# Kernel tuning notes

Measured on AMD Instinct MI355X. Metric: run time of the kernel, lower is better.

## Reference

```python
import jax, jax.numpy as jnp
import numpy as np

V, D, U, L, B, T = 32000, 256, 512, 2, 16, 128


def _lstm_stack(x, mask, params):
    """Stacked LSTM over time-major x [T,B,D] with mask [T,B].
    Keras LSTMCell gate order i,f,g,o; masked steps carry previous h,c."""
    nb = x.shape[1]
    init = tuple((jnp.zeros((nb, U), x.dtype), jnp.zeros((nb, U), x.dtype)) for _ in params)

    def step(carry, inp):
        xt, mt = inp
        m = mt[:, None]
        new = []
        h_in = xt
        for (W, Uw, b), (h, c) in zip(params, carry):
            z = h_in @ W + h @ Uw + b          # [B, 4U]
            i, f, g, o = jnp.split(z, 4, axis=-1)
            c_new = jax.nn.sigmoid(f) * c + jax.nn.sigmoid(i) * jnp.tanh(g)
            h_new = jax.nn.sigmoid(o) * jnp.tanh(c_new)
            h_new = jnp.where(m, h_new, h)
            c_new = jnp.where(m, c_new, c)
            new.append((h_new, c_new))
            h_in = h_new
        return tuple(new), h_in

    _, ys = jax.lax.scan(step, init, (x, mask))
    return ys  # [T, B, U]


def setup_inputs() -> dict:
    key = jax.random.key(0)
    ks = jax.random.split(key, 16)
    s = 0.05
    seqs = jax.random.randint(ks[0], (B, T), 0, V)
    embed = jax.random.normal(ks[1], (V, D), dtype=jnp.float32) * 0.01

    def lstm_p(k, din):
        k1, k2 = jax.random.split(k)
        return (jax.random.normal(k1, (din, 4 * U), dtype=jnp.float32) * s,
                jax.random.normal(k2, (U, 4 * U), dtype=jnp.float32) * s,
                jnp.zeros((4 * U,), dtype=jnp.float32))

    fW0, fU0, fb0 = lstm_p(ks[2], D)
    fW1, fU1, fb1 = lstm_p(ks[3], U)
    bW0, bU0, bb0 = lstm_p(ks[4], D)
    bW1, bU1, bb1 = lstm_p(ks[5], U)
    Wp = jax.random.normal(ks[6], (2 * U, V), dtype=jnp.float32) * s
    bp = jnp.zeros((V,), dtype=jnp.float32)
    return {"seqs": seqs, "embed": embed,
            "fW0": fW0, "fU0": fU0, "fb0": fb0, "fW1": fW1, "fU1": fU1, "fb1": fb1,
            "bW0": bW0, "bU0": bU0, "bb0": bb0, "bW1": bW1, "bU1": bU1, "bb1": bb1,
            "Wp": Wp, "bp": bp}


def reference(seqs, embed, fW0, fU0, fb0, fW1, fU1, fb1,
              bW0, bU0, bb0, bW1, bU1, bb1, Wp, bp):
    emb = embed[seqs]                      # [B, T, D]
    mask = seqs != 0                       # mask_zero=True
    # forward LSTM over tokens 0..T-2
    fx = jnp.swapaxes(emb[:, :-1], 0, 1)   # [T-1, B, D]
    fm = jnp.swapaxes(mask[:, :-1], 0, 1)
    f = jnp.swapaxes(_lstm_stack(fx, fm, [(fW0, fU0, fb0), (fW1, fU1, fb1)]), 0, 1)  # [B,T-1,U]
    # backward LSTM (go_backwards): process tokens 1..T-1 reversed in time
    bx = jnp.swapaxes(emb[:, 1:][:, ::-1], 0, 1)
    bm = jnp.swapaxes(mask[:, 1:][:, ::-1], 0, 1)
    b = jnp.swapaxes(_lstm_stack(bx, bm, [(bW0, bU0, bb0), (bW1, bU1, bb1)]), 0, 1)  # reversed-time order
    b_rev = b[:, ::-1]                     # tf.reverse(b, axis=[1]) -> natural order
    o = jnp.concatenate([f[:, :-1], b_rev[:, 1:]], axis=-1)  # [B, T-2, 2U]
    word_logits = o @ Wp + bp              # [B, T-2, V]
    return word_logits
```

## Files before the change

kernel.cpp:

```cpp
#include <hip/hip_runtime.h>

#define VOCAB 32000
#define DIM   256
#define UN    512
#define TT    128
#define T1    126
#define NG    2048
#define NBLK  256

typedef __attribute__((ext_vector_type(8))) __bf16 bf16x8;
typedef __attribute__((ext_vector_type(4))) float  f32x4;

__device__ __forceinline__ unsigned short f2bf(float f) {
  union { float f; unsigned u; } v; v.f = f;
  unsigned r = (v.u + 0x7fffu + ((v.u >> 16) & 1u)) >> 16;
  return (unsigned short)r;
}
__device__ __forceinline__ float f4_get(const float4& v, int j) {
  return j == 0 ? v.x : j == 1 ? v.y : j == 2 ? v.z : v.w;
}
__device__ __forceinline__ void async16(const void* g, void* l) {
  __builtin_amdgcn_global_load_lds((const __attribute__((address_space(1))) void*)g,
                                   (__attribute__((address_space(3))) void*)l, 16, 0, 0);
}

__global__ __launch_bounds__(256) void k_gather(const int* __restrict__ seqs,
                                                const float* __restrict__ embed,
                                                float* __restrict__ emb) {
  int idx = blockIdx.x * 256 + threadIdx.x;
  int d4 = idx & 63, bt = idx >> 6;
  int tok = seqs[bt];
  ((float4*)emb)[idx] = ((const float4*)embed)[(size_t)tok * 64 + d4];
}

__global__ __launch_bounds__(256, 2) void k_zin(const float* __restrict__ emb,
    const float* __restrict__ fW0, const float* __restrict__ fb0,
    const float* __restrict__ bW0, const float* __restrict__ bb0,
    float* __restrict__ Z0) {
  __shared__ __align__(16) float xs[16 * 260];
  int bi = blockIdx.x;
  int jh  = bi & 1;
  int t   = (bi >> 1) % T1;
  int dir = (bi >> 1) / T1;
  int tim = dir ? (TT - 1) - t : t;
  const float* W    = dir ? bW0 : fW0;
  const float* bias = dir ? bb0 : fb0;
  int tid = threadIdx.x;
  #pragma unroll
  for (int i = 0; i < 4; ++i) {
    int fidx = i * 256 + tid;
    int b = fidx >> 6, k4 = fidx & 63;
    float4 v = ((const float4*)emb)[(size_t)(b * TT + tim) * 64 + k4];
    *(float4*)&xs[b * 260 + k4 * 4] = v;
  }
  __syncthreads();
  int j0 = jh * 1024 + tid;
  float acc[4][16];
  #pragma unroll
  for (int q = 0; q < 4; ++q) {
    float bv = bias[j0 + q * 256];
    #pragma unroll
    for (int b = 0; b < 16; ++b) acc[q][b] = bv;
  }
  #pragma unroll 2
  for (int k = 0; k < DIM; k += 4) {
    float4 xv[16];
    #pragma unroll
    for (int b = 0; b < 16; ++b) xv[b] = *(const float4*)&xs[b * 260 + k];
    #pragma unroll
    for (int kk = 0; kk < 4; ++kk) {
      float w[4];
      #pragma unroll
      for (int q = 0; q < 4; ++q) w[q] = W[(size_t)(k + kk) * NG + j0 + q * 256];
      #pragma unroll
      for (int q = 0; q < 4; ++q)
        #pragma unroll
        for (int b = 0; b < 16; ++b)
          acc[q][b] += f4_get(xv[b], kk) * w[q];
    }
  }
  float* out = Z0 + ((size_t)(dir * T1 + t) * 16) * NG;
  #pragma unroll
  for (int q = 0; q < 4; ++q)
    #pragma unroll
    for (int b = 0; b < 16; ++b)
      out[(size_t)b * NG + j0 + q * 256] = acc[q][b];
}

__global__ __launch_bounds__(256) void k_cast_wp(const float* __restrict__ Wp,
                                                 unsigned short* __restrict__ Bt) {
  __shared__ float tile[32][33];
  int bi = blockIdx.x;
  int kt = bi & 31, nt = bi >> 5;
  int k0 = kt * 32, n0 = nt * 32;
  int tid = threadIdx.x;
  int nl = tid & 31, kl = tid >> 5;
  #pragma unroll
  for (int i = 0; i < 4; ++i) {
    int k = kl + i * 8;
    tile[k][nl] = Wp[(size_t)(k0 + k) * VOCAB + n0 + nl];
  }
  __syncthreads();
  int kl2 = tid & 31, nl2 = tid >> 5;
  #pragma unroll
  for (int i = 0; i < 4; ++i) {
    int n = nl2 + i * 8;
    Bt[(size_t)(n0 + n) * 1024 + k0 + kl2] = f2bf(tile[kl2][n]);
  }
}

__global__ __launch_bounds__(256) void k_padA(unsigned short* __restrict__ A) {
  int idx = blockIdx.x * 256 + threadIdx.x;
  ((uint4*)(A + (size_t)2016 * 1024))[idx] = make_uint4(0u, 0u, 0u, 0u);
}


__device__ __forceinline__ void wait_epoch(const int* ep, int target) {
  if (threadIdx.x == 0) {
    while (__hip_atomic_load(ep, __ATOMIC_RELAXED, __HIP_MEMORY_SCOPE_AGENT) < target)
      __builtin_amdgcn_s_sleep(2);
  }
  __syncthreads();
}

__device__ __forceinline__ void signal_step(int* grp, int sub_idx, int s) {
  __builtin_amdgcn_s_waitcnt(0);
  __syncthreads();
  if (threadIdx.x == 0) {
    int old = __hip_atomic_fetch_add(grp + sub_idx * 32, 1,
                                     __ATOMIC_RELAXED, __HIP_MEMORY_SCOPE_AGENT);
    if (old == 8 * (s + 1) - 1) {
      int mold = __hip_atomic_fetch_add(grp + 256, 1,
                                        __ATOMIC_RELAXED, __HIP_MEMORY_SCOPE_AGENT);
      if (mold == 8 * (s + 1) - 1) {
        #pragma unroll
        for (int i = 0; i < 8; ++i)
          __hip_atomic_store(grp + 512 + i * 32, s + 1,
                             __ATOMIC_RELAXED, __HIP_MEMORY_SCOPE_AGENT);
      }
    }
  }
}

__device__ __forceinline__ void ldstage_regs(float4 (&v)[8], const float* __restrict__ src) {
  const int tid = threadIdx.x;
  #pragma unroll
  for (int i = 0; i < 8; ++i) {
    const int fidx = i * 256 + tid;
    const int b = fidx >> 7, k = (fidx & 127) * 4;
    v[i] = *(const float4*)&src[(size_t)b * 512 + k];
  }
}
__device__ __forceinline__ void ldswrite(float* xs, const float4 (&v)[8]) {
  const int tid = threadIdx.x;
  #pragma unroll
  for (int i = 0; i < 8; ++i) {
    const int fidx = i * 256 + tid;
    const int b = fidx >> 7, k = (fidx & 127) * 4;
    *(float4*)&xs[b * 640 + (k >> 4) * 20 + (k & 15)] = v[i];
  }
}

__device__ __forceinline__ void phase_acc(const float* xs, const float (&u)[4][16],
                                          float (&acc)[4][16], int kp) {
  const float* xb = xs + kp * 20;
  #pragma unroll
  for (int kk4 = 0; kk4 < 4; ++kk4) {
    float4 xv[16];
    #pragma unroll
    for (int b = 0; b < 16; ++b) xv[b] = *(const float4*)&xb[b * 640 + kk4 * 4];
    #pragma unroll
    for (int j = 0; j < 4; ++j)
      #pragma unroll
      for (int g = 0; g < 4; ++g) {
        float uv = u[g][kk4 * 4 + j];
        #pragma unroll
        for (int b = 0; b < 16; ++b) acc[g][b] += f4_get(xv[b], j) * uv;
      }
  }
}

template <int LAYER>
__device__ void recur_path(const int* __restrict__ seqs,
                           const float* __restrict__ Z0,
                           const float* __restrict__ P1,
                           const float* __restrict__ P2,
                           const float* __restrict__ b1,
                           float* __restrict__ H0,
                           float* __restrict__ h1,
                           unsigned short* __restrict__ A,
                           int* grp_own, int sub_idx,
                           const int* ep_own, const int* ep_l0,
                           float* xsA, float* xsB, float* red,
                           int dir, int u0)
{
  const int tid = threadIdx.x;
  const int kp = tid >> 3;
  const int unit = u0 + (tid & 7);
  float u1r[4][16], u2r[4][16];
  #pragma unroll
  for (int g = 0; g < 4; ++g)
    #pragma unroll
    for (int kk = 0; kk < 16; ++kk) {
      const int col = g * UN + unit;
      u1r[g][kk] = P1[(size_t)(kp * 16 + kk) * NG + col];
      if (LAYER) u2r[g][kk] = P2[(size_t)(kp * 16 + kk) * NG + col];
    }
  const int cu = tid & 7, cb = tid >> 3;
  const int un = u0 + cu;
  float b1r[4] = {0.f, 0.f, 0.f, 0.f};
  if (LAYER && tid < 128) {
    #pragma unroll
    for (int g = 0; g < 4; ++g) b1r[g] = b1[g * UN + un];
  }
  float hst = 0.f, cstate = 0.f;

  for (int t = 0; t < 126; ++t) {
    float zp[4] = {0.f, 0.f, 0.f, 0.f};
    bool m = false;
    if (tid < 128) {
      const int tim = dir ? (TT - 1) - t : t;
      m = seqs[cb * TT + tim] != 0;
      if (LAYER == 0) {
        const float* zr = Z0 + (((size_t)dir * T1 + t) * 16 + cb) * NG;
        #pragma unroll
        for (int g = 0; g < 4; ++g) zp[g] = zr[g * UN + un];
      }
    }
    if (LAYER == 0) {
      float4 va[8];
      if (t == 0) {
        #pragma unroll
        for (int i = 0; i < 8; ++i) va[i] = make_float4(0.f, 0.f, 0.f, 0.f);
      } else {
        wait_epoch(ep_own, t);
        ldstage_regs(va, H0 + ((size_t)(dir * T1 + (t - 1)) * 16) * UN);
      }
      ldswrite(xsA, va);
    } else {
      float4 va[8], vb[8];
      if (t >= 1) {
        wait_epoch(ep_own, t);
        ldstage_regs(vb, h1 + ((size_t)((t - 1) * 2 + dir) * 16) * UN);
      } else {
        #pragma unroll
        for (int i = 0; i < 8; ++i) vb[i] = make_float4(0.f, 0.f, 0.f, 0.f);
      }
      wait_epoch(ep_l0, t + 1);
      ldstage_regs(va, H0 + ((size_t)(dir * T1 + t) * 16) * UN);
      ldswrite(xsB, vb);
      ldswrite(xsA, va);
    }
    __syncthreads();

    float acc[4][16];
    #pragma unroll
    for (int g = 0; g < 4; ++g)
      #pragma unroll
      for (int b = 0; b < 16; ++b) acc[g][b] = 0.f;
    phase_acc(xsA, u1r, acc, kp);
    if (LAYER) phase_acc(xsB, u2r, acc, kp);

    #pragma unroll
    for (int g = 0; g < 4; ++g)
      #pragma unroll
      for (int b = 0; b < 16; ++b) {
        float v = acc[g][b];
        v += __shfl_xor(v, 8);
        v += __shfl_xor(v, 16);
        v += __shfl_xor(v, 32);
        acc[g][b] = v;
      }
    const int lane = tid & 63, wv = tid >> 6;
    if (lane < 8) {
      #pragma unroll
      for (int g = 0; g < 4; ++g)
        #pragma unroll
        for (int b = 0; b < 16; ++b)
          red[((wv * 8 + lane) * 4 + g) * 17 + b] = acc[g][b];
    }
    __syncthreads();

    if (tid < 128) {
      float z[4];
      #pragma unroll
      for (int g = 0; g < 4; ++g) {
        float v = red[(cu * 4 + g) * 17 + cb];
        #pragma unroll
        for (int w = 1; w < 4; ++w) v += red[((w * 8 + cu) * 4 + g) * 17 + cb];
        z[g] = v + (LAYER ? b1r[g] : zp[g]);
      }
      const float si = 1.f / (1.f + expf(-z[0]));
      const float sf = 1.f / (1.f + expf(-z[1]));
      const float tg = tanhf(z[2]);
      const float so = 1.f / (1.f + expf(-z[3]));
      const float cn = sf * cstate + si * tg;
      const float hn = so * tanhf(cn);
      const float hsel = m ? hn : hst;
      const float csel = m ? cn : cstate;
      cstate = csel; hst = hsel;
      if (LAYER == 0) {
        __hip_atomic_store(&H0[(((size_t)dir * T1 + t) * 16 + cb) * UN + un],
                           hsel, __ATOMIC_RELAXED, __HIP_MEMORY_SCOPE_AGENT);
      } else {
        __hip_atomic_store(&h1[(((size_t)t * 2 + dir) * 16 + cb) * UN + un],
                           hsel, __ATOMIC_RELAXED, __HIP_MEMORY_SCOPE_AGENT);
        const int row = dir ? (125 - t) : t;
        A[((size_t)cb * T1 + row) * 1024 + dir * UN + un] = f2bf(hsel);
      }
    }
    signal_step(grp_own, sub_idx, t);
  }
}

__global__ __launch_bounds__(256, 1) void k_recur(
    const int* __restrict__ seqs, const float* __restrict__ Z0,
    const float* __restrict__ fU0, const float* __restrict__ bU0,
    const float* __restrict__ fW1, const float* __restrict__ fU1, const float* __restrict__ fb1,
    const float* __restrict__ bW1, const float* __restrict__ bU1, const float* __restrict__ bb1,
    float* __restrict__ H0, float* __restrict__ h1, unsigned short* __restrict__ A,
    int* __restrict__ bar)
{
  __shared__ __align__(16) float xs[2][16 * 640];
  __shared__ float red[32 * 4 * 17];
  const int bi = blockIdx.x;
  const int dir = (bi >> 6) & 1;
  const int u0 = (bi & 63) * 8;
  const int gid = bi >> 6;
  int* grp_own = bar + gid * 1024;
  const int* ep_own = grp_own + 512 + (bi & 7) * 32;
  const int* ep_l0  = bar + dir * 1024 + 512 + (bi & 7) * 32;
  if ((bi >> 7) == 0)
    recur_path<0>(seqs, Z0, dir ? bU0 : fU0, nullptr, nullptr,
                  H0, h1, A, grp_own, bi & 7, ep_own, ep_l0,
                  xs[0], xs[1], red, dir, u0);
  else
    recur_path<1>(seqs, Z0, dir ? bW1 : fW1, dir ? bU1 : fU1, dir ? bb1 : fb1,
                  H0, h1, A, grp_own, bi & 7, ep_own, ep_l0,
                  xs[0], xs[1], red, dir, u0);
}

__global__ __launch_bounds__(256, 2) void k_proj(
    const unsigned short* __restrict__ Abf, const unsigned short* __restrict__ Bt,
    const float* __restrict__ bp, float* __restrict__ out)
{
  __shared__ unsigned short As[128 * 32];
  __shared__ unsigned short Bs[128 * 32];
  int bi = blockIdx.x;
  int mt = bi & 15, nt = bi >> 4;
  int m0 = mt * 128, n0 = nt * 128;
  int tid = threadIdx.x;
  int wv = tid >> 6, lane = tid & 63;
  int wm = wv & 1, wn = wv >> 1;
  f32x4 acc[4][4] = {};
  for (int kt = 0; kt < 32; ++kt) {
    int r0 = wv * 32;
    #pragma unroll
    for (int i = 0; i < 2; ++i) {
      int row = r0 + i * 16 + (lane >> 2);
      const unsigned short* ga = Abf + (size_t)(m0 + row) * 1024 + kt * 32 + (lane & 3) * 8;
      async16(ga, As + (r0 + i * 16) * 32);
      const unsigned short* gb = Bt + (size_t)(n0 + row) * 1024 + kt * 32 + (lane & 3) * 8;
      async16(gb, Bs + (r0 + i * 16) * 32);
    }
    __syncthreads();
    bf16x8 af[4], bf[4];
    #pragma unroll
    for (int i = 0; i < 4; ++i) {
      int m = wm * 64 + i * 16 + (lane & 15);
      af[i] = *(const bf16x8*)&As[m * 32 + (lane >> 4) * 8];
      int n = wn * 64 + i * 16 + (lane & 15);
      bf[i] = *(const bf16x8*)&Bs[n * 32 + (lane >> 4) * 8];
    }
    #pragma unroll
    for (int i = 0; i < 4; ++i)
      #pragma unroll
      for (int j = 0; j < 4; ++j)
        acc[i][j] = __builtin_amdgcn_mfma_f32_16x16x32_bf16(af[i], bf[j], acc[i][j], 0, 0, 0);
    __syncthreads();
  }
  #pragma unroll
  for (int j = 0; j < 4; ++j) {
    int col = n0 + wn * 64 + j * 16 + (lane & 15);
    float bv = bp[col];
    #pragma unroll
    for (int i = 0; i < 4; ++i) {
      int rbase = m0 + wm * 64 + i * 16 + (lane >> 4) * 4;
      #pragma unroll
      for (int r = 0; r < 4; ++r) {
        int row = rbase + r;
        if (row < 2016) out[(size_t)row * VOCAB + col] = acc[i][j][r] + bv;
      }
    }
  }
}

extern "C" void kernel_launch(void* const* d_in, const int* in_sizes, int n_in,
                              void* d_out, int out_size, void* d_ws, size_t ws_size,
                              hipStream_t stream)
{
  const int*   seqs  = (const int*)  d_in[0];
  const float* embed = (const float*)d_in[1];
  const float* fW0 = (const float*)d_in[2];
  const float* fU0 = (const float*)d_in[3];
  const float* fb0 = (const float*)d_in[4];
  const float* fW1 = (const float*)d_in[5];
  const float* fU1 = (const float*)d_in[6];
  const float* fb1 = (const float*)d_in[7];
  const float* bW0 = (const float*)d_in[8];
  const float* bU0 = (const float*)d_in[9];
  const float* bb0 = (const float*)d_in[10];
  const float* bW1 = (const float*)d_in[11];
  const float* bU1 = (const float*)d_in[12];
  const float* bb1 = (const float*)d_in[13];
  const float* Wp  = (const float*)d_in[14];
  const float* bp  = (const float*)d_in[15];
  float* out = (float*)d_out;

  char* ws = (char*)d_ws;
  float* emb   = (float*)(ws);
  float* Z0    = (float*)(ws + 2097152);
  float* H0    = (float*)(ws + 35127296);
  float* h1    = (float*)(ws + 43384832);
  unsigned short* A  = (unsigned short*)(ws + 51642368);
  unsigned short* Bt = (unsigned short*)(ws + 55836672);
  int* bar = (int*)(ws + 1048576);

  hipLaunchKernelGGL(k_gather, dim3(512), dim3(256), 0, stream, seqs, embed, emb);
  hipLaunchKernelGGL(k_zin, dim3(504), dim3(256), 0, stream, emb, fW0, fb0, bW0, bb0, Z0);
  hipLaunchKernelGGL(k_cast_wp, dim3(32000), dim3(256), 0, stream, Wp, Bt);
  hipLaunchKernelGGL(k_padA, dim3(16), dim3(256), 0, stream, A);
  hipMemsetAsync(bar, 0, 16384, stream);

  void* rargs[] = {(void*)&seqs, (void*)&Z0, (void*)&fU0, (void*)&bU0,
                   (void*)&fW1, (void*)&fU1, (void*)&fb1,
                   (void*)&bW1, (void*)&bU1, (void*)&bb1,
                   (void*)&H0, (void*)&h1, (void*)&A, (void*)&bar};
  hipError_t ce = hipLaunchCooperativeKernel((void*)k_recur, dim3(NBLK), dim3(256),
                                             rargs, 0, stream);
  if (ce != hipSuccess) {
    (void)hipGetLastError();
    hipLaunchKernelGGL(k_recur, dim3(NBLK), dim3(256), 0, stream,
                       seqs, Z0, fU0, bU0, fW1, fU1, fb1, bW1, bU1, bb1,
                       H0, h1, A, bar);
  }

  hipLaunchKernelGGL(k_proj, dim3(4000), dim3(256), 0, stream, A, Bt, bp, out);
}
```

Before: 2.088 ms.

## Fold layer-0 and layer-1 LSTM chains into 128 blocks with flat counters

The persistent recurrence kernel drops from 256 to 128 blocks. Each block now runs the layer-0 step for one direction and the layer-1 step for the other direction in the same time loop, holding three weight slices in registers. The two-level barrier counter (per-subgroup, then master) becomes a single 64-way counter per chain, and the spin-wait sleep is shortened. The aim is to cut barrier latency and participant count per step, at the cost of serialising two cell updates per block per step and raising register pressure.

After: 3.540 ms. +69.5%, slower.

```diff
diff --git a/kernel.cpp b/kernel.cpp
--- a/kernel.cpp
+++ b/kernel.cpp
@@ -6,7 +6,7 @@
 #define TT    128
 #define T1    126
 #define NG    2048
-#define NBLK  256
+#define NBLK  128
 
 typedef __attribute__((ext_vector_type(8))) __bf16 bf16x8;
 typedef __attribute__((ext_vector_type(4))) float  f32x4;
@@ -115,29 +115,36 @@
 }
 
 
-__device__ __forceinline__ void wait_epoch(const int* ep, int target) {
+__device__ __forceinline__ void wait1(const int* ep, int tgt) {
   if (threadIdx.x == 0) {
-    while (__hip_atomic_load(ep, __ATOMIC_RELAXED, __HIP_MEMORY_SCOPE_AGENT) < target)
-      __builtin_amdgcn_s_sleep(2);
+    while (__hip_atomic_load(ep, __ATOMIC_RELAXED, __HIP_MEMORY_SCOPE_AGENT) < tgt)
+      __builtin_amdgcn_s_sleep(1);
   }
   __syncthreads();
 }
 
-__device__ __forceinline__ void signal_step(int* grp, int sub_idx, int s) {
+__device__ __forceinline__ void wait2(const int* e1, int t1, const int* e2, int t2) {
+  if (threadIdx.x == 0) {
+    for (;;) {
+      int a = __hip_atomic_load(e1, __ATOMIC_RELAXED, __HIP_MEMORY_SCOPE_AGENT);
+      int b = __hip_atomic_load(e2, __ATOMIC_RELAXED, __HIP_MEMORY_SCOPE_AGENT);
+      if (a >= t1 && b >= t2) break;
+      __builtin_amdgcn_s_sleep(1);
+    }
+  }
+  __syncthreads();
+}
+
+__device__ __forceinline__ void signal_chain(int* cnt, int s) {
   __builtin_amdgcn_s_waitcnt(0);
   __syncthreads();
   if (threadIdx.x == 0) {
-    int old = __hip_atomic_fetch_add(grp + sub_idx * 32, 1,
-                                     __ATOMIC_RELAXED, __HIP_MEMORY_SCOPE_AGENT);
-    if (old == 8 * (s + 1) - 1) {
-      int mold = __hip_atomic_fetch_add(grp + 256, 1,
-                                        __ATOMIC_RELAXED, __HIP_MEMORY_SCOPE_AGENT);
-      if (mold == 8 * (s + 1) - 1) {
-        #pragma unroll
-        for (int i = 0; i < 8; ++i)
-          __hip_atomic_store(grp + 512 + i * 32, s + 1,
-                             __ATOMIC_RELAXED, __HIP_MEMORY_SCOPE_AGENT);
-      }
+    int old = __hip_atomic_fetch_add(cnt, 1, __ATOMIC_RELAXED, __HIP_MEMORY_SCOPE_AGENT);
+    if (old == 64 * (s + 1) - 1) {
+      #pragma unroll
+      for (int i = 0; i < 8; ++i)
+        __hip_atomic_store(cnt + 128 + i * 32, s + 1,
+                           __ATOMIC_RELAXED, __HIP_MEMORY_SCOPE_AGENT);
     }
   }
 }
@@ -180,136 +187,24 @@
   }
 }
 
-template <int LAYER>
-__device__ void recur_path(const int* __restrict__ seqs,
-                           const float* __restrict__ Z0,
-                           const float* __restrict__ P1,
-                           const float* __restrict__ P2,
-                           const float* __restrict__ b1,
-                           float* __restrict__ H0,
-                           float* __restrict__ h1,
-                           unsigned short* __restrict__ A,
-                           int* grp_own, int sub_idx,
-                           const int* ep_own, const int* ep_l0,
-                           float* xsA, float* xsB, float* red,
-                           int dir, int u0)
-{
-  const int tid = threadIdx.x;
-  const int kp = tid >> 3;
-  const int unit = u0 + (tid & 7);
-  float u1r[4][16], u2r[4][16];
+__device__ __forceinline__ void reduce_write(float (&acc)[4][16], float* red, int tid) {
   #pragma unroll
   for (int g = 0; g < 4; ++g)
     #pragma unroll
-    for (int kk = 0; kk < 16; ++kk) {
-      const int col = g * UN + unit;
-      u1r[g][kk] = P1[(size_t)(kp * 16 + kk) * NG + col];
-      if (LAYER) u2r[g][kk] = P2[(size_t)(kp * 16 + kk) * NG + col];
-    }
-  const int cu = tid & 7, cb = tid >> 3;
-  const int un = u0 + cu;
-  float b1r[4] = {0.f, 0.f, 0.f, 0.f};
-  if (LAYER && tid < 128) {
-    #pragma unroll
-    for (int g = 0; g < 4; ++g) b1r[g] = b1[g * UN + un];
-  }
-  float hst = 0.f, cstate = 0.f;
-
-  for (int t = 0; t < 126; ++t) {
-    float zp[4] = {0.f, 0.f, 0.f, 0.f};
-    bool m = false;
-    if (tid < 128) {
-      const int tim = dir ? (TT - 1) - t : t;
-      m = seqs[cb * TT + tim] != 0;
-      if (LAYER == 0) {
-        const float* zr = Z0 + (((size_t)dir * T1 + t) * 16 + cb) * NG;
-        #pragma unroll
-        for (int g = 0; g < 4; ++g) zp[g] = zr[g * UN + un];
-      }
-    }
-    if (LAYER == 0) {
-      float4 va[8];
-      if (t == 0) {
-        #pragma unroll
-        for (int i = 0; i < 8; ++i) va[i] = make_float4(0.f, 0.f, 0.f, 0.f);
-      } else {
-        wait_epoch(ep_own, t);
-        ldstage_regs(va, H0 + ((size_t)(dir * T1 + (t - 1)) * 16) * UN);
-      }
-      ldswrite(xsA, va);
-    } else {
-      float4 va[8], vb[8];
-      if (t >= 1) {
-        wait_epoch(ep_own, t);
-        ldstage_regs(vb, h1 + ((size_t)((t - 1) * 2 + dir) * 16) * UN);
-      } else {
-        #pragma unroll
-        for (int i = 0; i < 8; ++i) vb[i] = make_float4(0.f, 0.f, 0.f, 0.f);
-      }
-      wait_epoch(ep_l0, t + 1);
-      ldstage_regs(va, H0 + ((size_t)(dir * T1 + t) * 16) * UN);
-      ldswrite(xsB, vb);
-      ldswrite(xsA, va);
-    }
-    __syncthreads();
-
-    float acc[4][16];
+    for (int b = 0; b < 16; ++b) {
+      float v = acc[g][b];
+      v += __shfl_xor(v, 8);
+      v += __shfl_xor(v, 16);
+      v += __shfl_xor(v, 32);
+      acc[g][b] = v;
+    }
+  const int lane = tid & 63, wv = tid >> 6;
+  if (lane < 8) {
     #pragma unroll
     for (int g = 0; g < 4; ++g)
       #pragma unroll
-      for (int b = 0; b < 16; ++b) acc[g][b] = 0.f;
-    phase_acc(xsA, u1r, acc, kp);
-    if (LAYER) phase_acc(xsB, u2r, acc, kp);
-
-    #pragma unroll
-    for (int g = 0; g < 4; ++g)
-      #pragma unroll
-      for (int b = 0; b < 16; ++b) {
-        float v = acc[g][b];
-        v += __shfl_xor(v, 8);
-        v += __shfl_xor(v, 16);
-        v += __shfl_xor(v, 32);
-        acc[g][b] = v;
-      }
-    const int lane = tid & 63, wv = tid >> 6;
-    if (lane < 8) {
-      #pragma unroll
-      for (int g = 0; g < 4; ++g)
-        #pragma unroll
-        for (int b = 0; b < 16; ++b)
-          red[((wv * 8 + lane) * 4 + g) * 17 + b] = acc[g][b];
-    }
-    __syncthreads();
-
-    if (tid < 128) {
-      float z[4];
-      #pragma unroll
-      for (int g = 0; g < 4; ++g) {
-        float v = red[(cu * 4 + g) * 17 + cb];
-        #pragma unroll
-        for (int w = 1; w < 4; ++w) v += red[((w * 8 + cu) * 4 + g) * 17 + cb];
-        z[g] = v + (LAYER ? b1r[g] : zp[g]);
-      }
-      const float si = 1.f / (1.f + expf(-z[0]));
-      const float sf = 1.f / (1.f + expf(-z[1]));
-      const float tg = tanhf(z[2]);
-      const float so = 1.f / (1.f + expf(-z[3]));
-      const float cn = sf * cstate + si * tg;
-      const float hn = so * tanhf(cn);
-      const float hsel = m ? hn : hst;
-      const float csel = m ? cn : cstate;
-      cstate = csel; hst = hsel;
-      if (LAYER == 0) {
-        __hip_atomic_store(&H0[(((size_t)dir * T1 + t) * 16 + cb) * UN + un],
-                           hsel, __ATOMIC_RELAXED, __HIP_MEMORY_SCOPE_AGENT);
-      } else {
-        __hip_atomic_store(&h1[(((size_t)t * 2 + dir) * 16 + cb) * UN + un],
-                           hsel, __ATOMIC_RELAXED, __HIP_MEMORY_SCOPE_AGENT);
-        const int row = dir ? (125 - t) : t;
-        A[((size_t)cb * T1 + row) * 1024 + dir * UN + un] = f2bf(hsel);
-      }
-    }
-    signal_step(grp_own, sub_idx, t);
+      for (int b = 0; b < 16; ++b)
+        red[((wv * 8 + lane) * 4 + g) * 17 + b] = acc[g][b];
   }
 }
 
@@ -323,21 +218,149 @@
 {
   __shared__ __align__(16) float xs[2][16 * 640];
   __shared__ float red[32 * 4 * 17];
+  const int tid = threadIdx.x;
   const int bi = blockIdx.x;
-  const int dir = (bi >> 6) & 1;
+  const int c  = bi >> 6;
   const int u0 = (bi & 63) * 8;
-  const int gid = bi >> 6;
-  int* grp_own = bar + gid * 1024;
-  const int* ep_own = grp_own + 512 + (bi & 7) * 32;
-  const int* ep_l0  = bar + dir * 1024 + 512 + (bi & 7) * 32;
-  if ((bi >> 7) == 0)
-    recur_path<0>(seqs, Z0, dir ? bU0 : fU0, nullptr, nullptr,
-                  H0, h1, A, grp_own, bi & 7, ep_own, ep_l0,
-                  xs[0], xs[1], red, dir, u0);
-  else
-    recur_path<1>(seqs, Z0, dir ? bW1 : fW1, dir ? bU1 : fU1, dir ? bb1 : fb1,
-                  H0, h1, A, grp_own, bi & 7, ep_own, ep_l0,
-                  xs[0], xs[1], red, dir, u0);
+  const int a  = c;
+  const int bd = 1 - c;
+  int* cntA = bar + a * 1024;
+  int* cntB = bar + (2 + bd) * 1024;
+  const int rep = 128 + (bi & 7) * 32;
+  const int* epA   = cntA + rep;
+  const int* epL0b = bar + bd * 1024 + rep;
+  const int* epB   = cntB + rep;
+
+  const int kp = tid >> 3;
+  const int unit = u0 + (tid & 7);
+  const float* U0 = a  ? bU0 : fU0;
+  const float* W1 = bd ? bW1 : fW1;
+  const float* U1 = bd ? bU1 : fU1;
+  const float* B1 = bd ? bb1 : fb1;
+  float u0r[4][16], w1r[4][16], u1r[4][16];
+  #pragma unroll
+  for (int g = 0; g < 4; ++g)
+    #pragma unroll
+    for (int kk = 0; kk < 16; ++kk) {
+      const int col = g * UN + unit;
+      const size_t rowo = (size_t)(kp * 16 + kk) * NG;
+      u0r[g][kk] = U0[rowo + col];
+      w1r[g][kk] = W1[rowo + col];
+      u1r[g][kk] = U1[rowo + col];
+    }
+  const int cu = tid & 7, cb = tid >> 3;
+  const int un = u0 + cu;
+  float b1r[4] = {0.f, 0.f, 0.f, 0.f};
+  if (tid < 128) {
+    #pragma unroll
+    for (int g = 0; g < 4; ++g) b1r[g] = B1[g * UN + un];
+  }
+  float hA = 0.f, cA = 0.f, hB = 0.f, cB = 0.f;
+
+  for (int t = 0; t < 126; ++t) {
+    float zp[4] = {0.f, 0.f, 0.f, 0.f};
+    bool ma = false, mb = false;
+    if (tid < 128) {
+      ma = seqs[cb * TT + (a  ? (TT - 1) - t : t)] != 0;
+      mb = seqs[cb * TT + (bd ? (TT - 1) - t : t)] != 0;
+      const float* zr = Z0 + (((size_t)a * T1 + t) * 16 + cb) * NG;
+      #pragma unroll
+      for (int g = 0; g < 4; ++g) zp[g] = zr[g * UN + un];
+    }
+    {
+      float4 va[8];
+      if (t == 0) {
+        #pragma unroll
+        for (int i = 0; i < 8; ++i) va[i] = make_float4(0.f, 0.f, 0.f, 0.f);
+      } else {
+        wait1(epA, t);
+        ldstage_regs(va, H0 + ((size_t)(a * T1 + (t - 1)) * 16) * UN);
+      }
+      ldswrite(xs[0], va);
+    }
+    __syncthreads();
+    {
+      float acc[4][16];
+      #pragma unroll
+      for (int g = 0; g < 4; ++g)
+        #pragma unroll
+        for (int b = 0; b < 16; ++b) acc[g][b] = 0.f;
+      phase_acc(xs[0], u0r, acc, kp);
+      reduce_write(acc, red, tid);
+    }
+    __syncthreads();
+    if (tid < 128) {
+      float z[4];
+      #pragma unroll
+      for (int g = 0; g < 4; ++g) {
+        float v = red[(cu * 4 + g) * 17 + cb];
+        #pragma unroll
+        for (int w = 1; w < 4; ++w) v += red[((w * 8 + cu) * 4 + g) * 17 + cb];
+        z[g] = v + zp[g];
+      }
+      const float si = 1.f / (1.f + expf(-z[0]));
+      const float sf = 1.f / (1.f + expf(-z[1]));
+      const float tg = tanhf(z[2]);
+      const float so = 1.f / (1.f + expf(-z[3]));
+      const float cn = sf * cA + si * tg;
+      const float hn = so * tanhf(cn);
+      const float hsel = ma ? hn : hA;
+      cA = ma ? cn : cA; hA = hsel;
+      __hip_atomic_store(&H0[(((size_t)a * T1 + t) * 16 + cb) * UN + un],
+                         hsel, __ATOMIC_RELAXED, __HIP_MEMORY_SCOPE_AGENT);
+    }
+    signal_chain(cntA, t);
+
+    {
+      float4 va[8], vb[8];
+      if (t == 0) {
+        wait1(epL0b, 1);
+        #pragma unroll
+        for (int i = 0; i < 8; ++i) vb[i] = make_float4(0.f, 0.f, 0.f, 0.f);
+      } else {
+        wait2(epL0b, t + 1, epB, t);
+        ldstage_regs(vb, h1 + ((size_t)((t - 1) * 2 + bd) * 16) * UN);
+      }
+      ldstage_regs(va, H0 + ((size_t)(bd * T1 + t) * 16) * UN);
+      ldswrite(xs[1], vb);
+      ldswrite(xs[0], va);
+    }
+    __syncthreads();
+    {
+      float acc[4][16];
+      #pragma unroll
+      for (int g = 0; g < 4; ++g)
+        #pragma unroll
+        for (int b = 0; b < 16; ++b) acc[g][b] = 0.f;
+      phase_acc(xs[0], w1r, acc, kp);
+      phase_acc(xs[1], u1r, acc, kp);
+      reduce_write(acc, red, tid);
+    }
+    __syncthreads();
+    if (tid < 128) {
+      float z[4];
+      #pragma unroll
+      for (int g = 0; g < 4; ++g) {
+        float v = red[(cu * 4 + g) * 17 + cb];
+        #pragma unroll
+        for (int w = 1; w < 4; ++w) v += red[((w * 8 + cu) * 4 + g) * 17 + cb];
+        z[g] = v + b1r[g];
+      }
+      const float si = 1.f / (1.f + expf(-z[0]));
+      const float sf = 1.f / (1.f + expf(-z[1]));
+      const float tg = tanhf(z[2]);
+      const float so = 1.f / (1.f + expf(-z[3]));
+      const float cn = sf * cB + si * tg;
+      const float hn = so * tanhf(cn);
+      const float hsel = mb ? hn : hB;
+      cB = mb ? cn : cB; hB = hsel;
+      __hip_atomic_store(&h1[(((size_t)t * 2 + bd) * 16 + cb) * UN + un],
+                         hsel, __ATOMIC_RELAXED, __HIP_MEMORY_SCOPE_AGENT);
+      const int row = bd ? (125 - t) : t;
+      A[((size_t)cb * T1 + row) * 1024 + bd * UN + un] = f2bf(hsel);
+    }
+    signal_chain(cntB, t);
+  }
 }
 
 __global__ __launch_bounds__(256, 2) void k_proj(
```

## Replace hierarchical atomic counter barrier with per-block step tags polled by wavefront

Applied to the files above, without the earlier changes.

Replaces the two-level fetch-add counter barrier, where the last arriver published an epoch, with per-block tag slots. Each block stores its step number into two replicated tag arrays, and waiters poll all 64 tags of a chain with one wavefront using __all. This removes the serialized atomic read-modify-write chain and the extra hop through a master counter from each recurrent step's critical path. Layer 1 now waits on both dependencies in a single combined poll. The cost is more polling traffic on global memory and a larger barrier memset.

Result: no change. 2.120 ms (+1.5%).

```diff
diff --git a/kernel.cpp b/kernel.cpp
--- a/kernel.cpp
+++ b/kernel.cpp
@@ -115,30 +115,37 @@
 }
 
 
-__device__ __forceinline__ void wait_epoch(const int* ep, int target) {
-  if (threadIdx.x == 0) {
-    while (__hip_atomic_load(ep, __ATOMIC_RELAXED, __HIP_MEMORY_SCOPE_AGENT) < target)
+__device__ __forceinline__ void wait_tags1(const int* tags, int tgt) {
+  if (threadIdx.x < 64) {
+    const int* p = tags + threadIdx.x * 32;
+    while (!__all(__hip_atomic_load(p, __ATOMIC_RELAXED,
+                                    __HIP_MEMORY_SCOPE_AGENT) >= tgt))
       __builtin_amdgcn_s_sleep(2);
   }
   __syncthreads();
 }
 
-__device__ __forceinline__ void signal_step(int* grp, int sub_idx, int s) {
+__device__ __forceinline__ void wait_tags2(const int* tA, int tgtA,
+                                           const int* tB, int tgtB) {
+  if (threadIdx.x < 64) {
+    const int* pa = tA + threadIdx.x * 32;
+    const int* pb = tB + threadIdx.x * 32;
+    for (;;) {
+      int a = __hip_atomic_load(pa, __ATOMIC_RELAXED, __HIP_MEMORY_SCOPE_AGENT);
+      int b = __hip_atomic_load(pb, __ATOMIC_RELAXED, __HIP_MEMORY_SCOPE_AGENT);
+      if (__all(a >= tgtA && b >= tgtB)) break;
+      __builtin_amdgcn_s_sleep(2);
+    }
+  }
+  __syncthreads();
+}
+
+__device__ __forceinline__ void signal_tags(int* t0, int* t1, int val) {
   __builtin_amdgcn_s_waitcnt(0);
   __syncthreads();
   if (threadIdx.x == 0) {
-    int old = __hip_atomic_fetch_add(grp + sub_idx * 32, 1,
-                                     __ATOMIC_RELAXED, __HIP_MEMORY_SCOPE_AGENT);
-    if (old == 8 * (s + 1) - 1) {
-      int mold = __hip_atomic_fetch_add(grp + 256, 1,
-                                        __ATOMIC_RELAXED, __HIP_MEMORY_SCOPE_AGENT);
-      if (mold == 8 * (s + 1) - 1) {
-        #pragma unroll
-        for (int i = 0; i < 8; ++i)
-          __hip_atomic_store(grp + 512 + i * 32, s + 1,
-                             __ATOMIC_RELAXED, __HIP_MEMORY_SCOPE_AGENT);
-      }
-    }
+    __hip_atomic_store(t0, val, __ATOMIC_RELAXED, __HIP_MEMORY_SCOPE_AGENT);
+    __hip_atomic_store(t1, val, __ATOMIC_RELAXED, __HIP_MEMORY_SCOPE_AGENT);
   }
 }
 
@@ -189,8 +196,8 @@
                            float* __restrict__ H0,
                            float* __restrict__ h1,
                            unsigned short* __restrict__ A,
-                           int* grp_own, int sub_idx,
-                           const int* ep_own, const int* ep_l0,
+                           int* tag0, int* tag1,
+                           const int* tags_own, const int* tags_l0,
                            float* xsA, float* xsB, float* red,
                            int dir, int u0)
 {
@@ -233,23 +240,24 @@
         #pragma unroll
         for (int i = 0; i < 8; ++i) va[i] = make_float4(0.f, 0.f, 0.f, 0.f);
       } else {
-        wait_epoch(ep_own, t);
+        wait_tags1(tags_own, t);
         ldstage_regs(va, H0 + ((size_t)(dir * T1 + (t - 1)) * 16) * UN);
       }
       ldswrite(xsA, va);
     } else {
       float4 va[8], vb[8];
-      if (t >= 1) {
-        wait_epoch(ep_own, t);
+      if (t == 0) {
+        wait_tags1(tags_l0, 1);
+        ldstage_regs(va, H0 + ((size_t)(dir * T1 + 0) * 16) * UN);
+        #pragma unroll
+        for (int i = 0; i < 8; ++i) vb[i] = make_float4(0.f, 0.f, 0.f, 0.f);
+      } else {
+        wait_tags2(tags_l0, t + 1, tags_own, t);
+        ldstage_regs(va, H0 + ((size_t)(dir * T1 + t) * 16) * UN);
         ldstage_regs(vb, h1 + ((size_t)((t - 1) * 2 + dir) * 16) * UN);
-      } else {
-        #pragma unroll
-        for (int i = 0; i < 8; ++i) vb[i] = make_float4(0.f, 0.f, 0.f, 0.f);
-      }
-      wait_epoch(ep_l0, t + 1);
-      ldstage_regs(va, H0 + ((size_t)(dir * T1 + t) * 16) * UN);
+      }
+      ldswrite(xsA, va);
       ldswrite(xsB, vb);
-      ldswrite(xsA, va);
     }
     __syncthreads();
 
@@ -309,7 +317,7 @@
         A[((size_t)cb * T1 + row) * 1024 + dir * UN + un] = f2bf(hsel);
       }
     }
-    signal_step(grp_own, sub_idx, t);
+    signal_tags(tag0, tag1, t + 1);
   }
 }
 
@@ -327,16 +335,20 @@
   const int dir = (bi >> 6) & 1;
   const int u0 = (bi & 63) * 8;
   const int gid = bi >> 6;
-  int* grp_own = bar + gid * 1024;
-  const int* ep_own = grp_own + 512 + (bi & 7) * 32;
-  const int* ep_l0  = bar + dir * 1024 + 512 + (bi & 7) * 32;
+  const int slot = bi & 63;
+  int* chain_own = bar + gid * 4096;
+  int* tag0 = chain_own + slot * 32;
+  int* tag1 = chain_own + 2048 + slot * 32;
+  const int rep = (bi & 1) * 2048;
+  const int* tags_own = chain_own + rep;
+  const int* tags_l0  = bar + dir * 4096 + rep;
   if ((bi >> 7) == 0)
     recur_path<0>(seqs, Z0, dir ? bU0 : fU0, nullptr, nullptr,
-                  H0, h1, A, grp_own, bi & 7, ep_own, ep_l0,
+                  H0, h1, A, tag0, tag1, tags_own, tags_l0,
                   xs[0], xs[1], red, dir, u0);
   else
     recur_path<1>(seqs, Z0, dir ? bW1 : fW1, dir ? bU1 : fU1, dir ? bb1 : fb1,
-                  H0, h1, A, grp_own, bi & 7, ep_own, ep_l0,
+                  H0, h1, A, tag0, tag1, tags_own, tags_l0,
                   xs[0], xs[1], red, dir, u0);
 }
 
@@ -430,7 +442,7 @@
   hipLaunchKernelGGL(k_zin, dim3(504), dim3(256), 0, stream, emb, fW0, fb0, bW0, bb0, Z0);
   hipLaunchKernelGGL(k_cast_wp, dim3(32000), dim3(256), 0, stream, Wp, Bt);
   hipLaunchKernelGGL(k_padA, dim3(16), dim3(256), 0, stream, A);
-  hipMemsetAsync(bar, 0, 16384, stream);
+  hipMemsetAsync(bar, 0, 65536, stream);
 
   void* rargs[] = {(void*)&seqs, (void*)&Z0, (void*)&fU0, (void*)&bU0,
                    (void*)&fW1, (void*)&fU1, (void*)&fb1,
```
